# Kernel optimization log

Measured on AMD Instinct MI355X. Metric: run time of the kernel, lower is better.

## Reference

```python
import jax, jax.numpy as jnp
import numpy as np

B, C, E, S, L, N = 2, 256, 256, 3, 5, 128
HMAX = 128
LEVEL_SIZES = np.array([128, 64, 32, 16, 8])
STRIDES = np.array([8.0, 16.0, 32.0, 64.0, 128.0])
GROUPS = 8
EPS = 1e-5


def setup_inputs() -> dict:
    key = jax.random.key(0)
    ks = jax.random.split(key, 16)
    # Padded FPN pyramid stacked as [L, B, C, HMAX, HMAX]; level l valid in [:sz, :sz]
    fm = jnp.zeros((L, B, C, HMAX, HMAX), jnp.float32)
    for l in range(L):
        sz = int(LEVEL_SIZES[l])
        fm = fm.at[l, :, :, :sz, :sz].set(jax.random.normal(ks[l], (B, C, sz, sz), jnp.float32))
    # Boxes in 1024x1024 image coordinates (x1, y1, x2, y2)
    cxy = jax.random.uniform(ks[5], (N, 2), minval=60.0, maxval=960.0)
    wh = jax.random.uniform(ks[6], (N, 2), minval=8.0, maxval=96.0)
    boxes = jnp.concatenate([cxy - wh / 2, cxy + wh / 2], axis=1)
    batch_idx = jax.random.randint(ks[7], (N,), 0, B, jnp.int32)
    level_idx = jax.random.randint(ks[8], (N,), 0, L, jnp.int32)
    sym_ids = jax.random.randint(ks[9], (N,), 0, 6, jnp.int32)
    conv_w = jax.random.normal(ks[10], (E, C, 3, 3), jnp.float32) / np.float32(np.sqrt(C * 9))
    gn_scale = jnp.ones((E,), jnp.float32)
    gn_bias = jnp.zeros((E,), jnp.float32)
    head_w = jax.random.normal(ks[11], (E, E), jnp.float32) / np.float32(np.sqrt(E))
    head_b = jnp.zeros((E,), jnp.float32)
    spat_w = jax.random.normal(ks[12], (E, 4), jnp.float32) * 0.01
    spat_b = jnp.zeros((E,), jnp.float32)
    sym_emb = jax.random.normal(ks[13], (6, E), jnp.float32) * 0.05
    fuse_w = jax.random.normal(ks[14], (6, E, E), jnp.float32) / np.float32(np.sqrt(E))
    fuse_b = jnp.zeros((6, E), jnp.float32)
    return dict(feature_maps=fm, boxes=boxes, conv_w=conv_w, gn_scale=gn_scale,
                gn_bias=gn_bias, head_w=head_w, head_b=head_b, spat_w=spat_w,
                spat_b=spat_b, sym_emb=sym_emb, fuse_w=fuse_w, fuse_b=fuse_b,
                batch_idx=batch_idx, level_idx=level_idx, sym_ids=sym_ids)


def _roi_align(fm, boxes, batch_idx, level_idx):
    # Batched roi_align (aligned=False, sampling_ratio=1) over all boxes at once.
    scale = (1.0 / jnp.asarray(STRIDES, fm.dtype))[level_idx]          # [N]
    hv = jnp.asarray(LEVEL_SIZES, fm.dtype)[level_idx]                 # [N] valid H=W per box
    x1 = boxes[:, 0] * scale; y1 = boxes[:, 1] * scale
    x2 = boxes[:, 2] * scale; y2 = boxes[:, 3] * scale
    roi_w = jnp.maximum(x2 - x1, 1.0)
    roi_h = jnp.maximum(y2 - y1, 1.0)
    off = (jnp.arange(S, dtype=fm.dtype) + 0.5) / S                    # bin centers
    xs = x1[:, None] + off[None, :] * roi_w[:, None]                   # [N,S]
    ys = y1[:, None] + off[None, :] * roi_h[:, None]                   # [N,S]
    y = jnp.broadcast_to(ys[:, :, None], (ys.shape[0], S, S))          # [N,S,S]
    x = jnp.broadcast_to(xs[:, None, :], (xs.shape[0], S, S))
    hvb = hv[:, None, None]
    valid = (y > -1.0) & (y < hvb) & (x > -1.0) & (x < hvb)
    yc = jnp.clip(y, 0.0, hvb - 1.0)
    xc = jnp.clip(x, 0.0, hvb - 1.0)
    y0 = jnp.floor(yc).astype(jnp.int32)
    x0 = jnp.floor(xc).astype(jnp.int32)
    hi = (hvb - 1.0).astype(jnp.int32)
    y1i = jnp.minimum(y0 + 1, hi)
    x1i = jnp.minimum(x0 + 1, hi)
    ly = yc - y0.astype(fm.dtype)
    lx = xc - x0.astype(fm.dtype)
    lvl = level_idx[:, None, None]
    bix = batch_idx[:, None, None]

    def g(yi, xi):
        # gather only the 4 corner pixels -> [N,S,S,C]
        return fm[lvl, bix, :, yi, xi]

    v = ((1 - ly) * (1 - lx))[..., None] * g(y0, x0) \
      + ((1 - ly) * lx)[..., None] * g(y0, x1i) \
      + (ly * (1 - lx))[..., None] * g(y1i, x0) \
      + (ly * lx)[..., None] * g(y1i, x1i)
    v = jnp.where(valid[..., None], v, 0.0)
    return jnp.transpose(v, (0, 3, 1, 2))                              # [N,C,S,S]


def _forward(feature_maps, boxes, conv_w, gn_scale, gn_bias, head_w, head_b,
             spat_w, spat_b, sym_emb, fuse_w, fuse_b, batch_idx, level_idx, sym_ids):
    roi = _roi_align(feature_maps, boxes, batch_idx, level_idx)        # [N,C,S,S]
    h = jax.lax.conv_general_dilated(roi, conv_w, (1, 1), ((1, 1), (1, 1)),
                                     dimension_numbers=('NCHW', 'OIHW', 'NCHW'))  # [N,E,S,S]
    n = h.shape[0]
    hg = h.reshape(n, GROUPS, -1)
    mu = hg.mean(-1, keepdims=True)
    var = hg.var(-1, keepdims=True)
    hg = (hg - mu) * jax.lax.rsqrt(var + EPS)
    h = hg.reshape(h.shape) * gn_scale[None, :, None, None] + gn_bias[None, :, None, None]
    h = jax.nn.relu(h)
    h = h.reshape(n, E, -1).mean(-1)                                   # spatial mean -> [N,E]
    head_out = jax.nn.relu(h @ head_w.T + head_b)                      # sym_feat_nn + ReLU
    spat = jax.nn.relu(boxes @ spat_w.T + spat_b)                      # spatial_embeddings
    fused_in = head_out + spat + sym_emb[sym_ids]                      # + class embedding
    out = jax.nn.relu(jnp.einsum('ne,nfe->nf', fused_in, fuse_w[sym_ids]) + fuse_b[sym_ids])
    return out                                                          # [N,E]


def reference(feature_maps, boxes, conv_w, gn_scale, gn_bias, head_w, head_b,
              spat_w, spat_b, sym_emb, fuse_w, fuse_b, batch_idx, level_idx, sym_ids):
    return _forward(feature_maps, boxes, conv_w, gn_scale, gn_bias, head_w, head_b,
                    spat_w, spat_b, sym_emb, fuse_w, fuse_b, batch_idx, level_idx, sym_ids)
```

## Files before the change

### kernel.cpp

```cpp
#include <hip/hip_runtime.h>
#include <hip/hip_bf16.h>


__global__ void t_f32(const float* __restrict__ in, float* __restrict__ out,
                      int rows, int cols) {
    __shared__ float tile[32][33];
    size_t mat = (size_t)blockIdx.z * rows * cols;
    int bx = blockIdx.x * 32, by = blockIdx.y * 32;
    int tx = threadIdx.x, ty = threadIdx.y;
#pragma unroll
    for (int i = 0; i < 32; i += 8) {
        int r = by + ty + i, c = bx + tx;
        if (r < rows && c < cols) tile[ty + i][tx] = in[mat + (size_t)r * cols + c];
    }
    __syncthreads();
#pragma unroll
    for (int i = 0; i < 32; i += 8) {
        int r = bx + ty + i, c = by + tx;
        if (r < cols && c < rows) out[mat + (size_t)r * rows + c] = tile[tx][ty + i];
    }
}

__global__ void t_bf16(const float* __restrict__ in, __hip_bfloat16* __restrict__ out,
                       int rows, int cols) {
    __shared__ float tile[32][33];
    int bx = blockIdx.x * 32, by = blockIdx.y * 32;
    int tx = threadIdx.x, ty = threadIdx.y;
#pragma unroll
    for (int i = 0; i < 32; i += 8) {
        int r = by + ty + i, c = bx + tx;
        if (r < rows && c < cols) tile[ty + i][tx] = in[(size_t)r * cols + c];
    }
    __syncthreads();
#pragma unroll
    for (int i = 0; i < 32; i += 8) {
        int r = bx + ty + i, c = by + tx;
        if (r < cols && c < rows) out[(size_t)r * rows + c] = __float2bfloat16(tile[tx][ty + i]);
    }
}

__global__ __launch_bounds__(256) void roi_align_k(
    const float* __restrict__ fm, const float* __restrict__ boxes,
    const int* __restrict__ batch_idx, const int* __restrict__ level_idx,
    float* __restrict__ roiT) {
    int blk = blockIdx.x;
    int n = blk / 9, p = blk % 9;
    int i = p / 3, j = p % 3;
    int c = threadIdx.x;

    int lvl = level_idx[n];
    int b = batch_idx[n];
    const float sizes[5]  = {128.f, 64.f, 32.f, 16.f, 8.f};
    const float invstr[5] = {1.f/8.f, 1.f/16.f, 1.f/32.f, 1.f/64.f, 1.f/128.f};
    float scale = invstr[lvl];
    float hv = sizes[lvl];

    float x1 = boxes[n*4+0] * scale, y1 = boxes[n*4+1] * scale;
    float x2 = boxes[n*4+2] * scale, y2 = boxes[n*4+3] * scale;
    float rw = fmaxf(x2 - x1, 1.f), rh = fmaxf(y2 - y1, 1.f);
    float x = x1 + (((float)j + 0.5f) / 3.f) * rw;
    float y = y1 + (((float)i + 0.5f) / 3.f) * rh;

    bool valid = (y > -1.f) && (y < hv) && (x > -1.f) && (x < hv);
    float yc = fminf(fmaxf(y, 0.f), hv - 1.f);
    float xc = fminf(fmaxf(x, 0.f), hv - 1.f);
    int y0 = (int)floorf(yc), x0 = (int)floorf(xc);
    int hi = (int)(hv - 1.f);
    int y1i = min(y0 + 1, hi), x1i = min(x0 + 1, hi);
    float ly = yc - (float)y0, lx = xc - (float)x0;

    const float* base = fm + (((size_t)lvl * 2 + b) * 256 + c) * (128 * 128);
    float v00 = base[y0 * 128 + x0];
    float v01 = base[y0 * 128 + x1i];
    float v10 = base[y1i * 128 + x0];
    float v11 = base[y1i * 128 + x1i];
    float v = (1.f - ly) * (1.f - lx) * v00 + (1.f - ly) * lx * v01 +
              ly * (1.f - lx) * v10 + ly * lx * v11;
    roiT[((size_t)n * 9 + p) * 256 + c] = valid ? v : 0.f;
}

__global__ __launch_bounds__(512) void conv_gn_pool(
    const float* __restrict__ roiT, const __hip_bfloat16* __restrict__ w_t,
    const float* __restrict__ gn_scale, const float* __restrict__ gn_bias,
    float* __restrict__ pooled) {
    __shared__ float lds_roi[256 * 12];
    __shared__ float red[2 * 128 * 9];

    int n  = blockIdx.x >> 1;
    int eh = blockIdx.x & 1;
    int t = threadIdx.x;
    int e_loc = t & 127;
    int ch = t >> 7;
    int e = eh * 128 + e_loc;

    const float* rsrc = roiT + (size_t)n * 2304;
    for (int v = t; v < 2304; v += 512) {
        int p = v >> 8, c = v & 255;
        lds_roi[c * 12 + p] = rsrc[v];
    }
    __syncthreads();

    float acc[9];
#pragma unroll
    for (int p = 0; p < 9; ++p) acc[p] = 0.f;

    int c0 = ch * 64;
    for (int c = c0; c < c0 + 64; ++c) {
        float r[9];
#pragma unroll
        for (int jj = 0; jj < 9; ++jj) r[jj] = lds_roi[c * 12 + jj];
        const __hip_bfloat16* wr = w_t + (size_t)c * 9 * 256 + e;
#pragma unroll
        for (int ky = 0; ky < 3; ++ky) {
#pragma unroll
            for (int kx = 0; kx < 3; ++kx) {
                float wv = __bfloat162float(wr[(ky * 3 + kx) * 256]);
#pragma unroll
                for (int oy = 0; oy < 3; ++oy) {
                    int iy = oy + ky - 1;
                    if (iy < 0 || iy > 2) continue;
#pragma unroll
                    for (int ox = 0; ox < 3; ++ox) {
                        int ix = ox + kx - 1;
                        if (ix < 0 || ix > 2) continue;
                        acc[oy * 3 + ox] = fmaf(wv, r[iy * 3 + ix], acc[oy * 3 + ox]);
                    }
                }
            }
        }
    }

    if (ch >= 2) {
#pragma unroll
        for (int p = 0; p < 9; ++p) red[((ch - 2) * 128 + e_loc) * 9 + p] = acc[p];
    }
    __syncthreads();
    if (ch < 2) {
#pragma unroll
        for (int p = 0; p < 9; ++p) acc[p] += red[(ch * 128 + e_loc) * 9 + p];
    }
    __syncthreads();
    if (ch == 1) {
#pragma unroll
        for (int p = 0; p < 9; ++p) red[e_loc * 9 + p] = acc[p];
    }
    __syncthreads();
    if (ch == 0) {
#pragma unroll
        for (int p = 0; p < 9; ++p) acc[p] += red[e_loc * 9 + p];

        float s = 0.f, sq = 0.f;
#pragma unroll
        for (int p = 0; p < 9; ++p) { s += acc[p]; sq += acc[p] * acc[p]; }
#pragma unroll
        for (int m = 16; m >= 1; m >>= 1) {
            s  += __shfl_xor(s, m, 64);
            sq += __shfl_xor(sq, m, 64);
        }
        float mean = s * (1.f / 288.f);
        float var = sq * (1.f / 288.f) - mean * mean;
        float rinv = rsqrtf(var + 1e-5f);
        float gs = gn_scale[e], gb = gn_bias[e];
        float ps = 0.f;
#pragma unroll
        for (int p = 0; p < 9; ++p) {
            float v = (acc[p] - mean) * rinv * gs + gb;
            ps += fmaxf(v, 0.f);
        }
        pooled[(size_t)n * 256 + e] = ps * (1.f / 9.f);
    }
}

__global__ __launch_bounds__(256) void head_fuse(
    const float* __restrict__ pooled, const float* __restrict__ boxes,
    const float* __restrict__ head_wT, const float* __restrict__ head_b,
    const float* __restrict__ spat_w, const float* __restrict__ spat_b,
    const float* __restrict__ sym_emb,
    const float* __restrict__ fuse_wT, const float* __restrict__ fuse_b,
    const int* __restrict__ sym_ids, float* __restrict__ out) {
    __shared__ float pl[256];
    __shared__ float fin[256];
    int n = blockIdx.x;
    int t = threadIdx.x;
    int sid = sym_ids[n];

    pl[t] = pooled[(size_t)n * 256 + t];
    __syncthreads();

    float acc = head_b[t];
#pragma unroll 4
    for (int k = 0; k < 256; ++k) acc = fmaf(pl[k], head_wT[k * 256 + t], acc);
    float ho = fmaxf(acc, 0.f);

    float4 sw = ((const float4*)spat_w)[t];
    float b0 = boxes[n*4+0], b1 = boxes[n*4+1], b2 = boxes[n*4+2], b3 = boxes[n*4+3];
    float sp = fmaxf(spat_b[t] + b0*sw.x + b1*sw.y + b2*sw.z + b3*sw.w, 0.f);

    fin[t] = ho + sp + sym_emb[sid * 256 + t];
    __syncthreads();

    float o = fuse_b[sid * 256 + t];
    const float* fw = fuse_wT + (size_t)sid * 65536;
#pragma unroll 4
    for (int k = 0; k < 256; ++k) o = fmaf(fin[k], fw[k * 256 + t], o);
    out[(size_t)n * 256 + t] = fmaxf(o, 0.f);
}

extern "C" void kernel_launch(void* const* d_in, const int* in_sizes, int n_in,
                              void* d_out, int out_size, void* d_ws, size_t ws_size,
                              hipStream_t stream) {
    const float* fm      = (const float*)d_in[0];
    const float* boxes   = (const float*)d_in[1];
    const float* conv_w  = (const float*)d_in[2];
    const float* gn_s    = (const float*)d_in[3];
    const float* gn_b    = (const float*)d_in[4];
    const float* head_w  = (const float*)d_in[5];
    const float* head_b  = (const float*)d_in[6];
    const float* spat_w  = (const float*)d_in[7];
    const float* spat_b  = (const float*)d_in[8];
    const float* sym_emb = (const float*)d_in[9];
    const float* fuse_w  = (const float*)d_in[10];
    const float* fuse_b  = (const float*)d_in[11];
    const int* batch_idx = (const int*)d_in[12];
    const int* level_idx = (const int*)d_in[13];
    const int* sym_ids   = (const int*)d_in[14];
    float* outp = (float*)d_out;

    char* ws = (char*)d_ws;
    __hip_bfloat16* w_t = (__hip_bfloat16*)ws;
    float* head_wT = (float*)(ws + 1179648);
    float* fuse_wT = (float*)(ws + 1441792);
    float* roiT    = (float*)(ws + 3014656);
    float* pooled  = (float*)(ws + 4194304);

    t_bf16<<<dim3(72, 8, 1), dim3(32, 8), 0, stream>>>(conv_w, w_t, 256, 2304);
    t_f32 <<<dim3(8, 8, 1),  dim3(32, 8), 0, stream>>>(head_w, head_wT, 256, 256);
    t_f32 <<<dim3(8, 8, 6),  dim3(32, 8), 0, stream>>>(fuse_w, fuse_wT, 256, 256);
    roi_align_k<<<1152, 256, 0, stream>>>(fm, boxes, batch_idx, level_idx, roiT);
    conv_gn_pool<<<256, 512, 0, stream>>>(roiT, w_t, gn_s, gn_b, pooled);
    head_fuse<<<128, 256, 0, stream>>>(pooled, boxes, head_wT, head_b, spat_w, spat_b,
                                       sym_emb, fuse_wT, fuse_b, sym_ids, outp);
}
```

Before: 299.5 us.

## Pack conv weights for vector loads, split conv across more blocks, merge transposes

Conv weights are repacked per (channel, output) as one 16-byte block of eight bf16 taps plus a separate ninth tap. The inner conv loop can then fetch all taps with one vector load instead of nine strided scalar loads. The conv/GN kernel now uses four 64-output blocks per ROI instead of two, with eight input-channel slices reduced in three steps through shared memory, to get more blocks running. The head and fuse weight transposes are merged into one launch, and the head matmul loops are unrolled further. The cost is an extra reduction stage and a weight-prep kernel whose global reads are strided.

After: 273.6 us. -8.7%, faster.

```diff
diff --git a/kernel.cpp b/kernel.cpp
--- a/kernel.cpp
+++ b/kernel.cpp
@@ -2,41 +2,40 @@
 #include <hip/hip_bf16.h>
 
 
-__global__ void t_f32(const float* __restrict__ in, float* __restrict__ out,
-                      int rows, int cols) {
+__device__ __forceinline__ float bf_lo(unsigned u) { return __uint_as_float(u << 16); }
+__device__ __forceinline__ float bf_hi(unsigned u) { return __uint_as_float(u & 0xffff0000u); }
+__device__ __forceinline__ unsigned short f2bf(float f) {
+    __hip_bfloat16 h = __float2bfloat16(f);
+    return *(unsigned short*)&h;
+}
+
+__global__ __launch_bounds__(256) void w_prep(const float* __restrict__ conv_w,
+                                              unsigned short* __restrict__ w8,
+                                              unsigned short* __restrict__ w9) {
+    int c = blockIdx.x, e = threadIdx.x;
+    const float* src = conv_w + ((size_t)e * 256 + c) * 9;
+    unsigned short tmp[8];
+#pragma unroll
+    for (int k = 0; k < 8; ++k) tmp[k] = f2bf(src[k]);
+    ((uint4*)w8)[(size_t)c * 256 + e] = *(const uint4*)tmp;
+    w9[(size_t)c * 256 + e] = f2bf(src[8]);
+}
+
+__global__ void t7(const float* __restrict__ head_w, const float* __restrict__ fuse_w,
+                   float* __restrict__ head_wT, float* __restrict__ fuse_wT) {
     __shared__ float tile[32][33];
-    size_t mat = (size_t)blockIdx.z * rows * cols;
+    int z = blockIdx.z;
+    const float* in = (z == 0) ? head_w : fuse_w + (size_t)(z - 1) * 65536;
+    float* out = (z == 0) ? head_wT : fuse_wT + (size_t)(z - 1) * 65536;
     int bx = blockIdx.x * 32, by = blockIdx.y * 32;
     int tx = threadIdx.x, ty = threadIdx.y;
 #pragma unroll
-    for (int i = 0; i < 32; i += 8) {
-        int r = by + ty + i, c = bx + tx;
-        if (r < rows && c < cols) tile[ty + i][tx] = in[mat + (size_t)r * cols + c];
-    }
-    __syncthreads();
-#pragma unroll
-    for (int i = 0; i < 32; i += 8) {
-        int r = bx + ty + i, c = by + tx;
-        if (r < cols && c < rows) out[mat + (size_t)r * rows + c] = tile[tx][ty + i];
-    }
-}
-
-__global__ void t_bf16(const float* __restrict__ in, __hip_bfloat16* __restrict__ out,
-                       int rows, int cols) {
-    __shared__ float tile[32][33];
-    int bx = blockIdx.x * 32, by = blockIdx.y * 32;
-    int tx = threadIdx.x, ty = threadIdx.y;
-#pragma unroll
-    for (int i = 0; i < 32; i += 8) {
-        int r = by + ty + i, c = bx + tx;
-        if (r < rows && c < cols) tile[ty + i][tx] = in[(size_t)r * cols + c];
-    }
-    __syncthreads();
-#pragma unroll
-    for (int i = 0; i < 32; i += 8) {
-        int r = bx + ty + i, c = by + tx;
-        if (r < cols && c < rows) out[(size_t)r * rows + c] = __float2bfloat16(tile[tx][ty + i]);
-    }
+    for (int i = 0; i < 32; i += 8)
+        tile[ty + i][tx] = in[(size_t)(by + ty + i) * 256 + bx + tx];
+    __syncthreads();
+#pragma unroll
+    for (int i = 0; i < 32; i += 8)
+        out[(size_t)(bx + ty + i) * 256 + by + tx] = tile[tx][ty + i];
 }
 
 __global__ __launch_bounds__(256) void roi_align_k(
@@ -79,19 +78,20 @@
     roiT[((size_t)n * 9 + p) * 256 + c] = valid ? v : 0.f;
 }
 
-__global__ __launch_bounds__(512) void conv_gn_pool(
-    const float* __restrict__ roiT, const __hip_bfloat16* __restrict__ w_t,
+__global__ __launch_bounds__(512, 2) void conv_gn_pool(
+    const float* __restrict__ roiT,
+    const unsigned short* __restrict__ w8, const unsigned short* __restrict__ w9,
     const float* __restrict__ gn_scale, const float* __restrict__ gn_bias,
     float* __restrict__ pooled) {
     __shared__ float lds_roi[256 * 12];
-    __shared__ float red[2 * 128 * 9];
-
-    int n  = blockIdx.x >> 1;
-    int eh = blockIdx.x & 1;
+    __shared__ float red[4 * 64 * 9];
+
+    int n  = blockIdx.x >> 2;
+    int eq = blockIdx.x & 3;
     int t = threadIdx.x;
-    int e_loc = t & 127;
-    int ch = t >> 7;
-    int e = eh * 128 + e_loc;
+    int e_loc = t & 63;
+    int ch = t >> 6;
+    int e = eq * 64 + e_loc;
 
     const float* rsrc = roiT + (size_t)n * 2304;
     for (int v = t; v < 2304; v += 512) {
@@ -104,17 +104,24 @@
 #pragma unroll
     for (int p = 0; p < 9; ++p) acc[p] = 0.f;
 
-    int c0 = ch * 64;
-    for (int c = c0; c < c0 + 64; ++c) {
+    int c0 = ch * 32;
+    for (int c = c0; c < c0 + 32; ++c) {
         float r[9];
 #pragma unroll
         for (int jj = 0; jj < 9; ++jj) r[jj] = lds_roi[c * 12 + jj];
-        const __hip_bfloat16* wr = w_t + (size_t)c * 9 * 256 + e;
+        uint4 wa = ((const uint4*)w8)[(size_t)c * 256 + e];
+        unsigned short w9v = w9[(size_t)c * 256 + e];
+        float wv[9];
+        wv[0] = bf_lo(wa.x); wv[1] = bf_hi(wa.x);
+        wv[2] = bf_lo(wa.y); wv[3] = bf_hi(wa.y);
+        wv[4] = bf_lo(wa.z); wv[5] = bf_hi(wa.z);
+        wv[6] = bf_lo(wa.w); wv[7] = bf_hi(wa.w);
+        wv[8] = bf_lo((unsigned)w9v);
 #pragma unroll
         for (int ky = 0; ky < 3; ++ky) {
 #pragma unroll
             for (int kx = 0; kx < 3; ++kx) {
-                float wv = __bfloat162float(wr[(ky * 3 + kx) * 256]);
+                float w = wv[ky * 3 + kx];
 #pragma unroll
                 for (int oy = 0; oy < 3; ++oy) {
                     int iy = oy + ky - 1;
@@ -123,21 +130,31 @@
                     for (int ox = 0; ox < 3; ++ox) {
                         int ix = ox + kx - 1;
                         if (ix < 0 || ix > 2) continue;
-                        acc[oy * 3 + ox] = fmaf(wv, r[iy * 3 + ix], acc[oy * 3 + ox]);
+                        acc[oy * 3 + ox] = fmaf(w, r[iy * 3 + ix], acc[oy * 3 + ox]);
                     }
                 }
             }
         }
     }
 
-    if (ch >= 2) {
-#pragma unroll
-        for (int p = 0; p < 9; ++p) red[((ch - 2) * 128 + e_loc) * 9 + p] = acc[p];
+    if (ch >= 4) {
+#pragma unroll
+        for (int p = 0; p < 9; ++p) red[((ch - 4) * 64 + e_loc) * 9 + p] = acc[p];
+    }
+    __syncthreads();
+    if (ch < 4) {
+#pragma unroll
+        for (int p = 0; p < 9; ++p) acc[p] += red[(ch * 64 + e_loc) * 9 + p];
+    }
+    __syncthreads();
+    if (ch >= 2 && ch < 4) {
+#pragma unroll
+        for (int p = 0; p < 9; ++p) red[((ch - 2) * 64 + e_loc) * 9 + p] = acc[p];
     }
     __syncthreads();
     if (ch < 2) {
 #pragma unroll
-        for (int p = 0; p < 9; ++p) acc[p] += red[(ch * 128 + e_loc) * 9 + p];
+        for (int p = 0; p < 9; ++p) acc[p] += red[(ch * 64 + e_loc) * 9 + p];
     }
     __syncthreads();
     if (ch == 1) {
@@ -188,7 +205,7 @@
     __syncthreads();
 
     float acc = head_b[t];
-#pragma unroll 4
+#pragma unroll 8
     for (int k = 0; k < 256; ++k) acc = fmaf(pl[k], head_wT[k * 256 + t], acc);
     float ho = fmaxf(acc, 0.f);
 
@@ -201,7 +218,7 @@
 
     float o = fuse_b[sid * 256 + t];
     const float* fw = fuse_wT + (size_t)sid * 65536;
-#pragma unroll 4
+#pragma unroll 8
     for (int k = 0; k < 256; ++k) o = fmaf(fin[k], fw[k * 256 + t], o);
     out[(size_t)n * 256 + t] = fmaxf(o, 0.f);
 }
@@ -227,17 +244,17 @@
     float* outp = (float*)d_out;
 
     char* ws = (char*)d_ws;
-    __hip_bfloat16* w_t = (__hip_bfloat16*)ws;
+    unsigned short* w8 = (unsigned short*)ws;
+    unsigned short* w9 = (unsigned short*)(ws + 1048576);
     float* head_wT = (float*)(ws + 1179648);
     float* fuse_wT = (float*)(ws + 1441792);
     float* roiT    = (float*)(ws + 3014656);
     float* pooled  = (float*)(ws + 4194304);
 
-    t_bf16<<<dim3(72, 8, 1), dim3(32, 8), 0, stream>>>(conv_w, w_t, 256, 2304);
-    t_f32 <<<dim3(8, 8, 1),  dim3(32, 8), 0, stream>>>(head_w, head_wT, 256, 256);
-    t_f32 <<<dim3(8, 8, 6),  dim3(32, 8), 0, stream>>>(fuse_w, fuse_wT, 256, 256);
+    w_prep<<<256, 256, 0, stream>>>(conv_w, w8, w9);
+    t7<<<dim3(8, 8, 7), dim3(32, 8), 0, stream>>>(head_w, fuse_w, head_wT, fuse_wT);
     roi_align_k<<<1152, 256, 0, stream>>>(fm, boxes, batch_idx, level_idx, roiT);
-    conv_gn_pool<<<256, 512, 0, stream>>>(roiT, w_t, gn_s, gn_b, pooled);
+    conv_gn_pool<<<512, 512, 0, stream>>>(roiT, w8, w9, gn_s, gn_b, pooled);
     head_fuse<<<128, 256, 0, stream>>>(pooled, boxes, head_wT, head_b, spat_w, spat_b,
                                        sym_emb, fuse_wT, fuse_b, sym_ids, outp);
 }
```
